# Performance work log

Measured on AMD Instinct MI355X. Metric: run time of the kernel, lower is better.

Reference implementation:

```python
import jax, jax.numpy as jnp
import numpy as np

N_NODES = 100000
N_FEAT = 128
DIM = 64
N_EDGES = 1600000
NNZ = 1000000
N_HE = 50000


def _gcn_conv(x, edge_index, W, b):
    n = x.shape[0]
    loop = jnp.arange(n)
    src = jnp.concatenate([edge_index[0], loop])
    dst = jnp.concatenate([edge_index[1], loop])
    deg = jax.ops.segment_sum(jnp.ones_like(dst, x.dtype), dst, num_segments=n)
    dinv = jnp.where(deg > 0, jax.lax.rsqrt(deg), 0.0)
    norm = dinv[src] * dinv[dst]
    xw = x @ W
    msg = xw[src] * norm[:, None]          # [E+n, dim] irregular gather
    return jax.ops.segment_sum(msg, dst, num_segments=n) + b


def _seg_mean(vals, idx, num_segments):
    s = jax.ops.segment_sum(vals, idx, num_segments=num_segments)
    c = jax.ops.segment_sum(jnp.ones_like(idx, vals.dtype), idx, num_segments=num_segments)
    return s / jnp.maximum(c, 1.0)[:, None]


def _equiv_set_gnn(x, hv, he, num_he, lin_in_W, lin_in_b, W1, b1, W2, b2, Wu, bu, cls_W, cls_b):
    # ED-HNN style EquivSetGNN: input MLP, one EquivSetConv layer (vertex->edge->vertex
    # mean aggregation with residual restart alpha=0.5), update MLP, classifier.
    ALPHA = 0.5
    h = jax.nn.relu(x @ lin_in_W + lin_in_b)          # [N, dim]
    h0 = h
    Xve = (h @ W1 + b1)[hv]                           # [nnz, dim] node -> incidence
    Xe = _seg_mean(Xve, he, num_he)                   # [num_he, dim] hyperedge features
    Xev = Xe[he]                                      # [nnz, dim]
    m = jax.nn.relu(jnp.concatenate([h[hv], Xev], axis=-1) @ W2 + b2)
    Xv = _seg_mean(m, hv, h.shape[0])                 # [N, dim]
    h = (1.0 - ALPHA) * Xv + ALPHA * h0
    h = jax.nn.relu(h @ Wu + bu)
    return h @ cls_W + cls_b


def setup_inputs() -> dict:
    key = jax.random.key(0)
    ks = jax.random.split(key, 20)
    s = 0.1
    inp = {
        "x": jax.random.normal(ks[0], (N_NODES, N_FEAT), jnp.float32),
        "edge_index": jax.random.randint(ks[1], (2, N_EDGES), 0, N_NODES),
        "hv": jax.random.randint(ks[2], (NNZ,), 0, N_NODES),
        "he": jax.random.randint(ks[3], (NNZ,), 0, N_HE),
        "num_hyperedges": N_HE,
        "conv1_W": s * jax.random.normal(ks[4], (N_FEAT, DIM), jnp.float32),
        "conv1_b": jnp.zeros((DIM,), jnp.float32),
        "conv2_W": s * jax.random.normal(ks[5], (DIM, DIM), jnp.float32),
        "conv2_b": jnp.zeros((DIM,), jnp.float32),
        "lin_in_W": s * jax.random.normal(ks[6], (N_FEAT, DIM), jnp.float32),
        "lin_in_b": jnp.zeros((DIM,), jnp.float32),
        "W1": s * jax.random.normal(ks[7], (DIM, DIM), jnp.float32),
        "b1": jnp.zeros((DIM,), jnp.float32),
        "W2": s * jax.random.normal(ks[8], (2 * DIM, DIM), jnp.float32),
        "b2": jnp.zeros((DIM,), jnp.float32),
        "Wu": s * jax.random.normal(ks[9], (DIM, DIM), jnp.float32),
        "bu": jnp.zeros((DIM,), jnp.float32),
        "cls_W": s * jax.random.normal(ks[10], (DIM, DIM), jnp.float32),
        "cls_b": jnp.zeros((DIM,), jnp.float32),
        "lp_W": s * jax.random.normal(ks[11], (2 * DIM, DIM), jnp.float32),
        "lp_b": jnp.zeros((DIM,), jnp.float32),
        "head_W": s * jax.random.normal(ks[12], (DIM, 1), jnp.float32),
        "head_b": jnp.zeros((1,), jnp.float32),
    }
    return inp


def reference(x, edge_index, hv, he, num_hyperedges,
              conv1_W, conv1_b, conv2_W, conv2_b,
              lin_in_W, lin_in_b, W1, b1, W2, b2, Wu, bu, cls_W, cls_b,
              lp_W, lp_b, head_W, head_b):
    # GCN branch (dropout is identity in eval mode)
    x_gnn = jax.nn.relu(_gcn_conv(x, edge_index, conv1_W, conv1_b))
    x_gnn = _gcn_conv(x_gnn, edge_index, conv2_W, conv2_b)
    # Hypergraph branch
    x_hyper = _equiv_set_gnn(x, hv, he, num_hyperedges,
                             lin_in_W, lin_in_b, W1, b1, W2, b2, Wu, bu, cls_W, cls_b)
    fused = jnp.concatenate([x_gnn, x_hyper], axis=-1) @ lp_W + lp_b
    out = (fused @ head_W + head_b).squeeze(-1)       # [N]
    return out
```

## Files before the change

kernel.cpp:

```cpp
#include <hip/hip_runtime.h>
#include <hip/hip_fp16.h>

#define NN 100000
#define NF 128
#define D  64
#define NE 1600000
#define NZ 1000000
#define NH 50000

#define NS (NN + NH + NN)
#define TOT (NE + 2 * NZ)
#define NBUK 977
#define NWG1 256
#define P2CAP 6144

typedef _Float16 half2v __attribute__((ext_vector_type(2)));

static __device__ __forceinline__ float waveReduceSum(float v) {
#pragma unroll
  for (int off = 32; off > 0; off >>= 1) v += __shfl_down(v, off);
  return v;
}

static __device__ __forceinline__ float bcastf(float v, int l) {
  return __int_as_float(__builtin_amdgcn_readlane(__float_as_int(v), l));
}

#if __has_builtin(__builtin_amdgcn_fdot2)
static __device__ __forceinline__ float fdot2f(half2v a, half2v b, float c) {
  return __builtin_amdgcn_fdot2(a, b, c, false);
}
#else
static __device__ __forceinline__ float fdot2f(half2v a, half2v b, float c) {
  return fmaf((float)a.x, (float)b.x, fmaf((float)a.y, (float)b.y, c));
}
#endif

__global__ void k_vecs(const float* __restrict__ conv2_W, const float* __restrict__ conv2_b,
                       const float* __restrict__ cls_W, const float* __restrict__ cls_b,
                       const float* __restrict__ lp_W, const float* __restrict__ lp_b,
                       const float* __restrict__ head_W, const float* __restrict__ head_b,
                       float* __restrict__ sv) {
  int t = threadIdx.x;
  __shared__ float v1[64], v2[64];
  float a1 = 0.f, a2 = 0.f;
  for (int c = 0; c < 64; ++c) {
    float hw = head_W[c];
    a1 = fmaf(lp_W[t * 64 + c], hw, a1);
    a2 = fmaf(lp_W[(64 + t) * 64 + c], hw, a2);
  }
  v1[t] = a1;
  v2[t] = a2;
  __syncthreads();
  float u = 0.f, w = 0.f;
  for (int c = 0; c < 64; ++c) {
    u = fmaf(conv2_W[t * 64 + c], v1[c], u);
    w = fmaf(cls_W[t * 64 + c], v2[c], w);
  }
  sv[t] = u;
  sv[64 + t] = w;
  float part = lp_b[t] * head_W[t] + conv2_b[t] * v1[t] + cls_b[t] * v2[t];
  part = waveReduceSum(part);
  if (t == 0) sv[128] = part + head_b[0];
}

__global__ void k_pack(const float* __restrict__ Wu, const float* __restrict__ W2,
                       int* __restrict__ WUP, int* __restrict__ W2P) {
  int t = blockIdx.x * 256 + threadIdx.x;
  if (t < 2048) {
    int kk = t >> 6, lane = t & 63;
    half2v p;
    p.x = (_Float16)Wu[(2 * kk) * 64 + lane];
    p.y = (_Float16)Wu[(2 * kk + 1) * 64 + lane];
    WUP[t] = __builtin_bit_cast(int, p);
  } else if (t < 4096) {
    int u = t - 2048;
    int kk = u >> 6, lane = u & 63;
    half2v p;
    p.x = (_Float16)W2[(64 + 2 * kk) * 64 + lane];
    p.y = (_Float16)W2[(64 + 2 * kk + 1) * 64 + lane];
    W2P[u] = __builtin_bit_cast(int, p);
  }
}

template <int K, bool BIAS, bool RELU, bool SCALE, typename IT, typename OT>
__global__ __launch_bounds__(256) void k_gemm(const IT* __restrict__ in,
                                              const float* __restrict__ W,
                                              const float* __restrict__ bias,
                                              const float* __restrict__ scale,
                                              OT* __restrict__ out, int nrows) {
  int lane = threadIdx.x & 63;
  int wave = threadIdx.x >> 6;
  float w[K];
#pragma unroll
  for (int k = 0; k < K; ++k) w[k] = W[k * 64 + lane];
  float b = BIAS ? bias[lane] : 0.0f;
  int wid = blockIdx.x * 4 + wave;
  int nw = gridDim.x * 4;
  if (wid >= nrows) return;
  float v0 = (float)in[(size_t)wid * K + lane];
  float v1 = 0.f;
  if constexpr (K == 128) v1 = (float)in[(size_t)wid * K + 64 + lane];
  for (int row = wid; row < nrows; row += nw) {
    int nrow = row + nw;
    float nv0 = 0.f, nv1 = 0.f;
    if (nrow < nrows) {
      nv0 = (float)in[(size_t)nrow * K + lane];
      if constexpr (K == 128) nv1 = (float)in[(size_t)nrow * K + 64 + lane];
    }
    float acc0 = b, acc1 = 0.f;
#pragma unroll
    for (int k = 0; k < 64; k += 2) {
      acc0 = fmaf(bcastf(v0, k), w[k], acc0);
      acc1 = fmaf(bcastf(v0, k + 1), w[k + 1], acc1);
    }
    if constexpr (K == 128) {
#pragma unroll
      for (int k = 0; k < 64; k += 2) {
        acc0 = fmaf(bcastf(v1, k), w[64 + k], acc0);
        acc1 = fmaf(bcastf(v1, k + 1), w[64 + k + 1], acc1);
      }
    }
    float r = acc0 + acc1;
    if (RELU) r = fmaxf(r, 0.0f);
    if (SCALE) r *= scale[row];
    out[(size_t)row * 64 + lane] = (OT)r;
    v0 = nv0;
    v1 = nv1;
  }
}

__global__ __launch_bounds__(256) void k_gemm_dual(const __half* __restrict__ in,
                                                   const float* __restrict__ W1,
                                                   const float* __restrict__ b1,
                                                   const float* __restrict__ W2,
                                                   __half* __restrict__ Cout,
                                                   __half* __restrict__ Aout, int nrows) {
  int lane = threadIdx.x & 63;
  int wave = threadIdx.x >> 6;
  float w1[64], w2[64];
#pragma unroll
  for (int k = 0; k < 64; ++k) {
    w1[k] = W1[k * 64 + lane];
    w2[k] = W2[k * 64 + lane];
  }
  float bb = b1[lane];
  int wid = blockIdx.x * 4 + wave;
  int nw = gridDim.x * 4;
  if (wid >= nrows) return;
  float v0 = (float)in[(size_t)wid * 64 + lane];
  for (int row = wid; row < nrows; row += nw) {
    int nrow = row + nw;
    float nv0 = (nrow < nrows) ? (float)in[(size_t)nrow * 64 + lane] : 0.f;
    float accC = bb, accA = 0.f;
#pragma unroll
    for (int k = 0; k < 64; ++k) {
      float f = bcastf(v0, k);
      accC = fmaf(f, w1[k], accC);
      accA = fmaf(f, w2[k], accA);
    }
    Cout[(size_t)row * 64 + lane] = (__half)accC;
    Aout[(size_t)row * 64 + lane] = (__half)accA;
    v0 = nv0;
  }
}

__global__ __launch_bounds__(1024) void k_phase1(const int* __restrict__ src,
                                                 const int* __restrict__ dst,
                                                 const int* __restrict__ he,
                                                 const int* __restrict__ hv,
                                                 int* __restrict__ gcur,
                                                 int* __restrict__ adj) {
  __shared__ int cnt[NBUK], base[NBUK], cur[NBUK];
  int tid = threadIdx.x;
  for (int b = tid; b < NBUK; b += 1024) { cnt[b] = 0; cur[b] = 0; }
  __syncthreads();
  int per = (TOT + NWG1 - 1) / NWG1;
  int s0 = blockIdx.x * per;
  int s1 = s0 + per; if (s1 > TOT) s1 = TOT;
  for (int j = s0 + tid; j < s1; j += 1024) {
    int id;
    if (j < NE) id = dst[j];
    else if (j < NE + NZ) id = NN + he[j - NE];
    else id = NN + NH + hv[j - NE - NZ];
    atomicAdd(&cnt[id >> 8], 1);
  }
  __syncthreads();
  for (int b = tid; b < NBUK; b += 1024) {
    int c = cnt[b];
    if (c) base[b] = b * P2CAP + atomicAdd(&gcur[b], c);
  }
  __syncthreads();
  for (int j = s0 + tid; j < s1; j += 1024) {
    int id, val;
    if (j < NE)           { id = dst[j];                val = src[j]; }
    else if (j < NE + NZ) { id = NN + he[j - NE];       val = hv[j - NE]; }
    else                  { id = NN + NH + hv[j - NE - NZ]; val = he[j - NE - NZ]; }
    int b = id >> 8;
    int slot = base[b] + atomicAdd(&cur[b], 1);
    adj[slot] = ((id & 255) << 17) | val;
  }
}

__global__ __launch_bounds__(256) void k_phase2(const int* __restrict__ gcur,
                                                int* __restrict__ adj,
                                                int* __restrict__ offb,
                                                int* __restrict__ offe) {
  __shared__ int ent[P2CAP];
  __shared__ int hist[256];
  int b = blockIdx.x, tid = threadIdx.x;
  int s = b * P2CAP;
  int n = gcur[b];
  if (n > P2CAP) n = P2CAP;
  hist[tid] = 0;
  __syncthreads();
  for (int k = tid; k < n; k += 256) {
    int v = adj[s + k];
    ent[k] = v;
    atomicAdd(&hist[v >> 17], 1);
  }
  __syncthreads();
  int c = hist[tid];
#pragma unroll
  for (int d = 1; d < 256; d <<= 1) {
    int x = (tid >= d) ? hist[tid - d] : 0;
    __syncthreads();
    hist[tid] += x;
    __syncthreads();
  }
  int excl = hist[tid] - c;
  hist[tid] = excl;
  int gid = (b << 8) + tid;
  if (gid < NS) {
    offb[gid] = s + excl;
    offe[gid] = s + excl + c;
  }
  __syncthreads();
  for (int k = tid; k < n; k += 256) {
    int v = ent[k];
    int pos = atomicAdd(&hist[v >> 17], 1);
    adj[s + pos] = v & 0x1FFFF;
  }
}

__global__ void k_dinv(const int* __restrict__ offb, const int* __restrict__ offe,
                       float* __restrict__ dinv) {
  int i = blockIdx.x * 256 + threadIdx.x;
  if (i < NN) dinv[i] = rsqrtf((float)(offe[i] - offb[i] + 1));
}

#define GATHER_PK16(ROWS2, PKBODY)                                      \
  for (int j0 = beg; j0 < end; j0 += 64) {                              \
    int m = end - j0; if (m > 64) m = 64;                               \
    int a = (lane < m) ? adj[j0 + lane] : 0;                            \
    for (int k = 0; k < m; k += 16) {                                   \
      int s_[8]; half2v r_[8];                                          \
      _Pragma("unroll")                                                 \
      for (int q = 0; q < 8; ++q) {                                     \
        int kk = k + 2 * q + eo;                                        \
        int kc = (kk < m - 1) ? kk : (m - 1);                           \
        s_[q] = __shfl(a, kc);                                          \
      }                                                                 \
      _Pragma("unroll")                                                 \
      for (int q = 0; q < 8; ++q) r_[q] = ROWS2[(size_t)s_[q] * 32 + c]; \
      half2v b2 = hz;                                                   \
      _Pragma("unroll")                                                 \
      for (int q = 0; q < 8; ++q) {                                     \
        bool ok = (k + 2 * q + eo) < m;                                 \
        PKBODY                                                          \
      }                                                                 \
      ax += (float)b2.x; ay += (float)b2.y;                             \
    }                                                                   \
  }

__global__ __launch_bounds__(256) void k_gcn1_gather(const int* __restrict__ offb,
                                                     const int* __restrict__ offe,
                                                     const int* __restrict__ adj,
                                                     const __half* __restrict__ xw1p,
                                                     const float* __restrict__ dinv,
                                                     const float* __restrict__ conv1_b,
                                                     const float* __restrict__ sv,
                                                     float* __restrict__ tp) {
  int i = blockIdx.x * 4 + (threadIdx.x >> 6);
  if (i >= NN) return;
  int lane = threadIdx.x & 63;
  int c = lane & 31, eo = lane >> 5;
  const half2v hz = {(_Float16)0.f, (_Float16)0.f};
  const half2v* X2 = (const half2v*)xw1p;
  int beg = offb[i], end = offe[i];
  float ax = 0.f, ay = 0.f;
  GATHER_PK16(X2, { b2 += ok ? r_[q] : hz; })
  ax += __shfl_xor(ax, 32);
  ay += __shfl_xor(ay, 32);
  float di = dinv[i];
  half2v self2 = X2[(size_t)i * 32 + c];
  float r0 = fmaxf(fmaf(ax + (float)self2.x, di, conv1_b[2 * c]), 0.f);
  float r1 = fmaxf(fmaf(ay + (float)self2.y, di, conv1_b[2 * c + 1]), 0.f);
  float p = r0 * sv[2 * c] + r1 * sv[2 * c + 1];
  if (eo) p = 0.f;
  p = waveReduceSum(p);
  if (lane == 0) tp[i] = p * di;
}

__global__ __launch_bounds__(256) void k_xe_gather(const int* __restrict__ offb,
                                                   const int* __restrict__ offe,
                                                   const int* __restrict__ adj,
                                                   const __half* __restrict__ C,
                                                   const int* __restrict__ W2P,
                                                   const float* __restrict__ b2bias,
                                                   __half* __restrict__ B) {
  __shared__ float hp[4][4][64];
  int lane = threadIdx.x & 63, wv = threadIdx.x >> 6;
  int c = lane & 31, eo = lane >> 5;
  const half2v hz = {(_Float16)0.f, (_Float16)0.f};
  const half2v* C2 = (const half2v*)C;
  int base = (blockIdx.x * 4 + wv) * 4;
  if (base >= NH) return;
  int ncnt = NH - base; if (ncnt > 4) ncnt = 4;
  for (int n = 0; n < ncnt; ++n) {
    int e = base + n;
    int beg = offb[NN + e], end = offe[NN + e];
    float ax = 0.f, ay = 0.f;
    GATHER_PK16(C2, { b2 += ok ? r_[q] : hz; })
    ax += __shfl_xor(ax, 32);
    ay += __shfl_xor(ay, 32);
    if (!eo) {
      float sc = 1.0f / fmaxf((float)(end - beg), 1.f);
      hp[wv][n][2 * c] = ax * sc;
      hp[wv][n][2 * c + 1] = ay * sc;
    }
  }
  __builtin_amdgcn_wave_barrier();
  int l2 = lane & 31;
  int hvp[4];
#pragma unroll
  for (int n = 0; n < 4; ++n) {
    half2v p;
    p.x = (_Float16)hp[wv][n][2 * l2];
    p.y = (_Float16)hp[wv][n][2 * l2 + 1];
    hvp[n] = __builtin_bit_cast(int, p);
  }
  float bb = b2bias[lane];
  float acc[4];
#pragma unroll
  for (int n = 0; n < 4; ++n) acc[n] = bb;
  for (int kk = 0; kk < 32; ++kk) {
    half2v wp = __builtin_bit_cast(half2v, W2P[kk * 64 + lane]);
#pragma unroll
    for (int n = 0; n < 4; ++n) {
      half2v hb = __builtin_bit_cast(half2v, __builtin_amdgcn_readlane(hvp[n], kk));
      acc[n] = fdot2f(hb, wp, acc[n]);
    }
  }
#pragma unroll
  for (int n = 0; n < 4; ++n)
    if (n < ncnt) B[(size_t)(base + n) * 64 + lane] = (__half)acc[n];
}

__global__ __launch_bounds__(256) void k_final(const int* __restrict__ offb,
                                               const int* __restrict__ offe,
                                               const int* __restrict__ adj,
                                               const __half* __restrict__ A,
                                               const __half* __restrict__ B,
                                               const __half* __restrict__ h,
                                               const float* __restrict__ tp,
                                               const float* __restrict__ dinv,
                                               const int* __restrict__ WUP,
                                               const float* __restrict__ bu,
                                               const float* __restrict__ sv,
                                               float* __restrict__ out) {
  __shared__ float hp[4][8][64];
  __shared__ float sarr[4][8];
  int lane = threadIdx.x & 63, wv = threadIdx.x >> 6;
  int c = lane & 31, eo = lane >> 5;
  const half2v hz = {(_Float16)0.f, (_Float16)0.f};
  const half2v* A2 = (const half2v*)A;
  const half2v* B2 = (const half2v*)B;
  const half2v* H2 = (const half2v*)h;
  int base = (blockIdx.x * 4 + wv) * 8;
  if (base >= NN) return;
  int ncnt = NN - base; if (ncnt > 8) ncnt = 8;
  float c_all = sv[128];
  for (int n = 0; n < ncnt; ++n) {
    int i = base + n;
    half2v av2 = A2[(size_t)i * 32 + c];
    int beg = offb[NN + NH + i], end = offe[NN + NH + i];
    float ax = 0.f, ay = 0.f;
    GATHER_PK16(B2, {
      half2v s = av2 + r_[q];
      s = __builtin_elementwise_max(s, hz);
      b2 += ok ? s : hz;
    })
    ax += __shfl_xor(ax, 32);
    ay += __shfl_xor(ay, 32);
    if (!eo) {
      float sc = 0.5f / fmaxf((float)(end - beg), 1.f);
      half2v h2 = H2[(size_t)i * 32 + c];
      hp[wv][n][2 * c] = ax * sc + 0.5f * (float)h2.x;
      hp[wv][n][2 * c + 1] = ay * sc + 0.5f * (float)h2.y;
    }
    float di = dinv[i];
    int db = offb[i], de = offe[i];
    float g = 0.f;
    for (int j = db + lane; j < de; j += 64) g += tp[adj[j]];
    float gr = waveReduceSum(g);
    if (lane == 0) sarr[wv][n] = gr * di + tp[i] * di + c_all;
  }
  __builtin_amdgcn_wave_barrier();
  int l2 = lane & 31;
  int hvp[8];
#pragma unroll
  for (int n = 0; n < 8; ++n) {
    half2v p;
    p.x = (_Float16)hp[wv][n][2 * l2];
    p.y = (_Float16)hp[wv][n][2 * l2 + 1];
    hvp[n] = __builtin_bit_cast(int, p);
  }
  float bb = bu[lane];
  float w2v = sv[64 + lane];
  float acc[8];
#pragma unroll
  for (int n = 0; n < 8; ++n) acc[n] = bb;
  for (int kk = 0; kk < 32; ++kk) {
    half2v wp = __builtin_bit_cast(half2v, WUP[kk * 64 + lane]);
#pragma unroll
    for (int n = 0; n < 8; ++n) {
      half2v hb = __builtin_bit_cast(half2v, __builtin_amdgcn_readlane(hvp[n], kk));
      acc[n] = fdot2f(hb, wp, acc[n]);
    }
  }
#pragma unroll
  for (int n = 0; n < 8; ++n) {
    if (n < ncnt) {
      float part = fmaxf(acc[n], 0.f) * w2v;
      float tot = waveReduceSum(part);
      if (lane == 0) out[base + n] = tot + sarr[wv][n];
    }
  }
}

extern "C" void kernel_launch(void* const* d_in, const int* in_sizes, int n_in,
                              void* d_out, int out_size, void* d_ws, size_t ws_size,
                              hipStream_t stream) {
  (void)in_sizes; (void)n_in; (void)out_size; (void)ws_size;
  const float* x       = (const float*)d_in[0];
  const int*   ei      = (const int*)d_in[1];
  const int*   hv      = (const int*)d_in[2];
  const int*   he      = (const int*)d_in[3];
  const float* conv1_W = (const float*)d_in[5];
  const float* conv1_b = (const float*)d_in[6];
  const float* conv2_W = (const float*)d_in[7];
  const float* conv2_b = (const float*)d_in[8];
  const float* lin_W   = (const float*)d_in[9];
  const float* lin_b   = (const float*)d_in[10];
  const float* W1      = (const float*)d_in[11];
  const float* b1      = (const float*)d_in[12];
  const float* W2      = (const float*)d_in[13];
  const float* b2      = (const float*)d_in[14];
  const float* Wu      = (const float*)d_in[15];
  const float* bu      = (const float*)d_in[16];
  const float* cls_W   = (const float*)d_in[17];
  const float* cls_b   = (const float*)d_in[18];
  const float* lp_W    = (const float*)d_in[19];
  const float* lp_b    = (const float*)d_in[20];
  const float* head_W  = (const float*)d_in[21];
  const float* head_b  = (const float*)d_in[22];
  const int* src = ei;
  const int* dst = ei + NE;
  float* out = (float*)d_out;

  __half* H16  = (__half*)d_ws;
  __half* PH   = H16 + (size_t)NN * 64;
  __half* QH   = PH + (size_t)NN * 64;
  __half* XEH  = QH + (size_t)NN * 64;
  float* DINV  = (float*)(XEH + (size_t)NH * 64);
  float* TP    = DINV + NN;
  float* SV    = TP + NN;
  int* WUP     = (int*)(SV + 192);
  int* W2P     = WUP + 2048;
  int* GCUR    = W2P + 2048;
  int* OFFB    = GCUR + NBUK;
  int* OFFE    = OFFB + NS;
  int* ADJ     = OFFE + NS;

  hipMemsetAsync(GCUR, 0, NBUK * 4, stream);

  k_vecs<<<1, 64, 0, stream>>>(conv2_W, conv2_b, cls_W, cls_b, lp_W, lp_b, head_W, head_b, SV);
  k_pack<<<16, 256, 0, stream>>>(Wu, W2, WUP, W2P);

  k_phase1<<<NWG1, 1024, 0, stream>>>(src, dst, he, hv, GCUR, ADJ);
  k_phase2<<<NBUK, 256, 0, stream>>>(GCUR, ADJ, OFFB, OFFE);
  k_dinv<<<(NN + 255) / 256, 256, 0, stream>>>(OFFB, OFFE, DINV);

  k_gemm<128, false, false, true, float, __half><<<2048, 256, 0, stream>>>(x, conv1_W, nullptr, DINV, PH, NN);
  k_gemm<128, true, true, false, float, __half><<<2048, 256, 0, stream>>>(x, lin_W, lin_b, nullptr, H16, NN);

  k_gcn1_gather<<<NN / 4, 256, 0, stream>>>(OFFB, OFFE, ADJ, PH, DINV, conv1_b, SV, TP);

  k_gemm_dual<<<2048, 256, 0, stream>>>(H16, W1, b1, W2, PH, QH, NN);

  k_xe_gather<<<3125, 256, 0, stream>>>(OFFB, OFFE, ADJ, PH, W2P, b2, XEH);

  k_final<<<3125, 256, 0, stream>>>(OFFB, OFFE, ADJ, QH, XEH, H16, TP, DINV, WUP, bu, SV, out);
}
```

Measured before the change: 357.9 us.

## Fuse two x-input GEMMs into one fp16 dot2 kernel with packed weights

Merges the conv1 and lin_in GEMMs over x into a single kernel, so x (100k×128 fp32) is read once instead of twice. Both that kernel and the W1/W2 dual GEMM now use packed half2 weights with fdot2 and readlane broadcasts, which halves the FMA count and the weight-register footprint. The weight packing kernel is extended to pre-convert the extra matrices. Converting x and the weights to fp16 before accumulating adds rounding error.

```diff
diff --git a/kernel.cpp b/kernel.cpp
--- a/kernel.cpp
+++ b/kernel.cpp
@@ -65,103 +65,104 @@
 }
 
 __global__ void k_pack(const float* __restrict__ Wu, const float* __restrict__ W2,
-                       int* __restrict__ WUP, int* __restrict__ W2P) {
+                       const float* __restrict__ conv1_W, const float* __restrict__ lin_W,
+                       const float* __restrict__ W1,
+                       int* __restrict__ PK) {
   int t = blockIdx.x * 256 + threadIdx.x;
-  if (t < 2048) {
-    int kk = t >> 6, lane = t & 63;
-    half2v p;
-    p.x = (_Float16)Wu[(2 * kk) * 64 + lane];
-    p.y = (_Float16)Wu[(2 * kk + 1) * 64 + lane];
-    WUP[t] = __builtin_bit_cast(int, p);
-  } else if (t < 4096) {
-    int u = t - 2048;
-    int kk = u >> 6, lane = u & 63;
-    half2v p;
-    p.x = (_Float16)W2[(64 + 2 * kk) * 64 + lane];
-    p.y = (_Float16)W2[(64 + 2 * kk + 1) * 64 + lane];
-    W2P[u] = __builtin_bit_cast(int, p);
-  }
-}
-
-template <int K, bool BIAS, bool RELU, bool SCALE, typename IT, typename OT>
-__global__ __launch_bounds__(256) void k_gemm(const IT* __restrict__ in,
-                                              const float* __restrict__ W,
-                                              const float* __restrict__ bias,
-                                              const float* __restrict__ scale,
-                                              OT* __restrict__ out, int nrows) {
+  if (t >= 16384) return;
+  const float* srcm;
+  int idx, roff = 0;
+  if (t < 2048)       { srcm = Wu;      idx = t;          }
+  else if (t < 4096)  { srcm = W2;      idx = t - 2048;  roff = 64; }
+  else if (t < 8192)  { srcm = conv1_W; idx = t - 4096;  }
+  else if (t < 12288) { srcm = lin_W;   idx = t - 8192;  }
+  else if (t < 14336) { srcm = W1;      idx = t - 12288; }
+  else                { srcm = W2;      idx = t - 14336; }
+  int kk = idx >> 6, lane = idx & 63;
+  half2v p;
+  p.x = (_Float16)srcm[(roff + 2 * kk) * 64 + lane];
+  p.y = (_Float16)srcm[(roff + 2 * kk + 1) * 64 + lane];
+  PK[t] = __builtin_bit_cast(int, p);
+}
+
+__global__ __launch_bounds__(256) void k_gemm128_dual(const float* __restrict__ x,
+                                                      const int* __restrict__ C1P,
+                                                      const int* __restrict__ LWP,
+                                                      const float* __restrict__ lin_b,
+                                                      const float* __restrict__ dinv,
+                                                      __half* __restrict__ xw1p,
+                                                      __half* __restrict__ h16, int nrows) {
   int lane = threadIdx.x & 63;
   int wave = threadIdx.x >> 6;
-  float w[K];
-#pragma unroll
-  for (int k = 0; k < K; ++k) w[k] = W[k * 64 + lane];
-  float b = BIAS ? bias[lane] : 0.0f;
+  int w1[64], w2[64];
+#pragma unroll
+  for (int k = 0; k < 64; ++k) {
+    w1[k] = C1P[k * 64 + lane];
+    w2[k] = LWP[k * 64 + lane];
+  }
+  float bb = lin_b[lane];
   int wid = blockIdx.x * 4 + wave;
   int nw = gridDim.x * 4;
   if (wid >= nrows) return;
-  float v0 = (float)in[(size_t)wid * K + lane];
-  float v1 = 0.f;
-  if constexpr (K == 128) v1 = (float)in[(size_t)wid * K + 64 + lane];
+  const float2* X2 = (const float2*)x;
+  float2 v = X2[(size_t)wid * 64 + lane];
   for (int row = wid; row < nrows; row += nw) {
     int nrow = row + nw;
-    float nv0 = 0.f, nv1 = 0.f;
-    if (nrow < nrows) {
-      nv0 = (float)in[(size_t)nrow * K + lane];
-      if constexpr (K == 128) nv1 = (float)in[(size_t)nrow * K + 64 + lane];
-    }
-    float acc0 = b, acc1 = 0.f;
-#pragma unroll
-    for (int k = 0; k < 64; k += 2) {
-      acc0 = fmaf(bcastf(v0, k), w[k], acc0);
-      acc1 = fmaf(bcastf(v0, k + 1), w[k + 1], acc1);
-    }
-    if constexpr (K == 128) {
-#pragma unroll
-      for (int k = 0; k < 64; k += 2) {
-        acc0 = fmaf(bcastf(v1, k), w[64 + k], acc0);
-        acc1 = fmaf(bcastf(v1, k + 1), w[64 + k + 1], acc1);
-      }
-    }
-    float r = acc0 + acc1;
-    if (RELU) r = fmaxf(r, 0.0f);
-    if (SCALE) r *= scale[row];
-    out[(size_t)row * 64 + lane] = (OT)r;
-    v0 = nv0;
-    v1 = nv1;
+    float2 nv = make_float2(0.f, 0.f);
+    if (nrow < nrows) nv = X2[(size_t)nrow * 64 + lane];
+    half2v hv;
+    hv.x = (_Float16)v.x;
+    hv.y = (_Float16)v.y;
+    int hvi = __builtin_bit_cast(int, hv);
+    float a0 = 0.f, a1 = bb;
+#pragma unroll
+    for (int kk = 0; kk < 64; ++kk) {
+      half2v xb = __builtin_bit_cast(half2v, __builtin_amdgcn_readlane(hvi, kk));
+      a0 = fdot2f(xb, __builtin_bit_cast(half2v, w1[kk]), a0);
+      a1 = fdot2f(xb, __builtin_bit_cast(half2v, w2[kk]), a1);
+    }
+    xw1p[(size_t)row * 64 + lane] = (__half)(a0 * dinv[row]);
+    h16[(size_t)row * 64 + lane] = (__half)fmaxf(a1, 0.f);
+    v = nv;
   }
 }
 
 __global__ __launch_bounds__(256) void k_gemm_dual(const __half* __restrict__ in,
-                                                   const float* __restrict__ W1,
+                                                   const int* __restrict__ W1P,
                                                    const float* __restrict__ b1,
-                                                   const float* __restrict__ W2,
+                                                   const int* __restrict__ W2AP,
                                                    __half* __restrict__ Cout,
                                                    __half* __restrict__ Aout, int nrows) {
   int lane = threadIdx.x & 63;
   int wave = threadIdx.x >> 6;
-  float w1[64], w2[64];
-#pragma unroll
-  for (int k = 0; k < 64; ++k) {
-    w1[k] = W1[k * 64 + lane];
-    w2[k] = W2[k * 64 + lane];
+  int w1[32], w2[32];
+#pragma unroll
+  for (int k = 0; k < 32; ++k) {
+    w1[k] = W1P[k * 64 + lane];
+    w2[k] = W2AP[k * 64 + lane];
   }
   float bb = b1[lane];
   int wid = blockIdx.x * 4 + wave;
   int nw = gridDim.x * 4;
   if (wid >= nrows) return;
-  float v0 = (float)in[(size_t)wid * 64 + lane];
+  const half2v* IN2 = (const half2v*)in;
+  int c32 = lane & 31;
+  half2v v = IN2[(size_t)wid * 32 + c32];
   for (int row = wid; row < nrows; row += nw) {
     int nrow = row + nw;
-    float nv0 = (nrow < nrows) ? (float)in[(size_t)nrow * 64 + lane] : 0.f;
+    half2v nv = {(_Float16)0.f, (_Float16)0.f};
+    if (nrow < nrows) nv = IN2[(size_t)nrow * 32 + c32];
+    int hvi = __builtin_bit_cast(int, v);
     float accC = bb, accA = 0.f;
 #pragma unroll
-    for (int k = 0; k < 64; ++k) {
-      float f = bcastf(v0, k);
-      accC = fmaf(f, w1[k], accC);
-      accA = fmaf(f, w2[k], accA);
+    for (int kk = 0; kk < 32; ++kk) {
+      half2v xb = __builtin_bit_cast(half2v, __builtin_amdgcn_readlane(hvi, kk));
+      accC = fdot2f(xb, __builtin_bit_cast(half2v, w1[kk]), accC);
+      accA = fdot2f(xb, __builtin_bit_cast(half2v, w2[kk]), accA);
     }
     Cout[(size_t)row * 64 + lane] = (__half)accC;
     Aout[(size_t)row * 64 + lane] = (__half)accA;
-    v0 = nv0;
+    v = nv;
   }
 }
 
@@ -476,9 +477,14 @@
   float* DINV  = (float*)(XEH + (size_t)NH * 64);
   float* TP    = DINV + NN;
   float* SV    = TP + NN;
-  int* WUP     = (int*)(SV + 192);
-  int* W2P     = WUP + 2048;
-  int* GCUR    = W2P + 2048;
+  int* PK      = (int*)(SV + 192);
+  int* WUP     = PK;
+  int* W2P     = PK + 2048;
+  int* C1P     = PK + 4096;
+  int* LWP     = PK + 8192;
+  int* W1P     = PK + 12288;
+  int* W2AP    = PK + 14336;
+  int* GCUR    = PK + 16384;
   int* OFFB    = GCUR + NBUK;
   int* OFFE    = OFFB + NS;
   int* ADJ     = OFFE + NS;
@@ -486,18 +492,17 @@
   hipMemsetAsync(GCUR, 0, NBUK * 4, stream);
 
   k_vecs<<<1, 64, 0, stream>>>(conv2_W, conv2_b, cls_W, cls_b, lp_W, lp_b, head_W, head_b, SV);
-  k_pack<<<16, 256, 0, stream>>>(Wu, W2, WUP, W2P);
+  k_pack<<<64, 256, 0, stream>>>(Wu, W2, conv1_W, lin_W, W1, PK);
 
   k_phase1<<<NWG1, 1024, 0, stream>>>(src, dst, he, hv, GCUR, ADJ);
   k_phase2<<<NBUK, 256, 0, stream>>>(GCUR, ADJ, OFFB, OFFE);
   k_dinv<<<(NN + 255) / 256, 256, 0, stream>>>(OFFB, OFFE, DINV);
 
-  k_gemm<128, false, false, true, float, __half><<<2048, 256, 0, stream>>>(x, conv1_W, nullptr, DINV, PH, NN);
-  k_gemm<128, true, true, false, float, __half><<<2048, 256, 0, stream>>>(x, lin_W, lin_b, nullptr, H16, NN);
+  k_gemm128_dual<<<2048, 256, 0, stream>>>(x, C1P, LWP, lin_b, DINV, PH, H16, NN);
 
   k_gcn1_gather<<<NN / 4, 256, 0, stream>>>(OFFB, OFFE, ADJ, PH, DINV, conv1_b, SV, TP);
 
-  k_gemm_dual<<<2048, 256, 0, stream>>>(H16, W1, b1, W2, PH, QH, NN);
+  k_gemm_dual<<<2048, 256, 0, stream>>>(H16, W1P, b1, W2AP, PH, QH, NN);
 
   k_xe_gather<<<3125, 256, 0, stream>>>(OFFB, OFFE, ADJ, PH, W2P, b2, XEH);
 
```

After: 296.5 us. 17.1% less time.
